# Optimization experiments

Hardware: AMD Instinct MI355X
Metric: run time of the kernel (lower is better)

## Reference

```python
import jax, jax.numpy as jnp
import numpy as np

NEG = -1e9  # finite stand-in for -inf so vjp stays NaN-free
BLANK = 28


def setup_inputs() -> dict:
    key = jax.random.key(0)
    k = jax.random.split(key, 6)
    B, T, D, V, L = 64, 1000, 512, 29, 200
    features = jax.random.normal(k[0], (B, T, D), jnp.float32)
    W = jax.random.normal(k[1], (D, V), jnp.float32) / np.sqrt(D)
    b = jnp.zeros((V,), jnp.float32)
    labels = jax.random.randint(k[2], (B, L), 0, BLANK)          # targets never use blank id
    feature_lengths = jax.random.randint(k[3], (B,), T // 2, T + 1)
    label_lengths = jax.random.randint(k[4], (B,), 50, L + 1)
    return dict(features=features, W=W, b=b, labels=labels,
                feature_lengths=feature_lengths, label_lengths=label_lengths)


def _ctc_loss(log_probs, labels, feature_lengths, label_lengths):
    # log_probs: [T, B, V] (already log_softmax'd)
    T, B, V = log_probs.shape
    L = labels.shape[1]
    S = 2 * L + 1  # extended label length (blanks interleaved)
    ext = jnp.full((B, S), BLANK, labels.dtype).at[:, 1::2].set(labels)  # [B,S]
    # skip transition s-2 -> s allowed iff ext[s] != blank and ext[s] != ext[s-2]
    ext_m2 = jnp.pad(ext[:, :-2], ((0, 0), (2, 0)), constant_values=BLANK)
    allow_skip = (ext != BLANK) & (ext != ext_m2)  # [B,S]
    # gather per-timestep log-probs of extended labels: [T,B,S]
    lp_ext = jnp.take_along_axis(log_probs, jnp.broadcast_to(ext[None], (T, B, S)), axis=2)
    # alpha trellis, t = 0
    alpha = (jnp.full((B, S), NEG, log_probs.dtype)
             .at[:, 0].set(lp_ext[0, :, 0])
             .at[:, 1].set(lp_ext[0, :, 1]))

    def step(alpha, inp):
        lp_t, t = inp  # lp_t: [B,S]
        a2 = jnp.pad(alpha[:, :-1], ((0, 0), (1, 0)), constant_values=NEG)
        a3 = jnp.where(allow_skip,
                       jnp.pad(alpha[:, :-2], ((0, 0), (2, 0)), constant_values=NEG),
                       NEG)
        new = lp_t + jnp.logaddexp(jnp.logaddexp(alpha, a2), a3)
        # freeze alpha once past this sample's input length
        new = jnp.where(t < feature_lengths[:, None], new, alpha)
        return new, None

    alpha, _ = jax.lax.scan(step, alpha, (lp_ext[1:], jnp.arange(1, T)))
    # final states: last blank (2*L_b) and last label (2*L_b - 1)
    idx_blank = 2 * label_lengths  # [B]
    l1 = jnp.take_along_axis(alpha, idx_blank[:, None], axis=1)[:, 0]
    l2 = jnp.take_along_axis(alpha, jnp.maximum(idx_blank - 1, 0)[:, None], axis=1)[:, 0]
    l2 = jnp.where(label_lengths > 0, l2, NEG)
    nll = -jnp.logaddexp(l1, l2)  # [B]
    # PyTorch reduction='mean': divide each loss by target length, then average.
    # zero_infinity=True: infeasible (effectively infinite) losses are zeroed.
    denom = jnp.maximum(label_lengths, 1).astype(log_probs.dtype)
    nll = jnp.where(nll < -0.5 * NEG, nll / denom, 0.0)
    return jnp.mean(nll)


def reference(features, W, b, labels, feature_lengths, label_lengths):
    # model head: Linear(D -> V), then log_softmax and (B,T,V) -> (T,B,V)
    logits = jnp.einsum('btd,dv->btv', features, W) + b
    log_probs = jax.nn.log_softmax(logits, axis=-1).transpose(1, 0, 2)
    return _ctc_loss(log_probs, labels, feature_lengths, label_lengths)
```

## Files before the change

### kernel.cpp

```cpp
#include <hip/hip_runtime.h>
#include <hip/hip_bf16.h>
#include <math.h>

#define B_  64
#define T_  1000
#define D_  512
#define V_  29
#define L_  200
#define S_  401
#define VPAD 32
#define BLANK_ 28

typedef __attribute__((ext_vector_type(8))) short short8v;
typedef __attribute__((ext_vector_type(4))) float float4v;

__device__ __forceinline__ unsigned short f2bf(float f) {
    unsigned int u = __float_as_uint(f);
    return (unsigned short)((u + 0x7FFFu + ((u >> 16) & 1u)) >> 16);
}

__global__ __launch_bounds__(256) void head_mfma_softmax_kernel(
    const float* __restrict__ feat,
    const float* __restrict__ W,
    const float* __restrict__ bias,
    const int*   __restrict__ flen,
    float*       __restrict__ p)
{
    __shared__ uint4 bfrag_lds[16 * 2 * 64];
    const int tid = threadIdx.x;

    for (int f = tid; f < 2048; f += 256) {
        int ks  = f >> 7;
        int rem = f & 127;
        int tl  = rem >> 6;
        int ln  = rem & 63;
        int k0  = ks * 32 + (ln >> 4) * 8;
        int col = tl * 16 + (ln & 15);
        unsigned short h[8];
        #pragma unroll
        for (int j = 0; j < 8; ++j) {
            float wv = (col < V_) ? W[(size_t)(k0 + j) * V_ + col] : 0.f;
            h[j] = f2bf(wv);
        }
        uint4 pk;
        pk.x = h[0] | ((unsigned)h[1] << 16);
        pk.y = h[2] | ((unsigned)h[3] << 16);
        pk.z = h[4] | ((unsigned)h[5] << 16);
        pk.w = h[6] | ((unsigned)h[7] << 16);
        bfrag_lds[f] = pk;
    }
    __syncthreads();

    const int wv  = tid >> 6;
    const int l   = tid & 63;
    const int c0  = l & 15;
    const int grp = l >> 4;
    const float bias0 = bias[c0];
    const bool  v1ok  = (c0 + 16) < V_;
    const float bias1 = v1ok ? bias[c0 + 16] : 0.f;

    #pragma unroll
    for (int ti = 0; ti < 2; ++ti) {
        const int tile = (blockIdx.x * 4 + wv) * 2 + ti;
        const int r0   = tile * 16;
        const int b0 = r0 / T_;
        const bool active = ((r0 - b0 * T_) < flen[b0]) || ((r0 + 15) / T_ != b0);
        if (!active) continue;

        const float* abase = feat + (size_t)(r0 + c0) * D_ + grp * 8;
        float4v acc0 = {0.f, 0.f, 0.f, 0.f};
        float4v acc1 = {0.f, 0.f, 0.f, 0.f};

        #pragma unroll 4
        for (int ks = 0; ks < 16; ++ks) {
            float4 fa = *(const float4*)(abase + ks * 32);
            float4 fb = *(const float4*)(abase + ks * 32 + 4);
            short8v a;
            a[0] = (short)f2bf(fa.x); a[1] = (short)f2bf(fa.y);
            a[2] = (short)f2bf(fa.z); a[3] = (short)f2bf(fa.w);
            a[4] = (short)f2bf(fb.x); a[5] = (short)f2bf(fb.y);
            a[6] = (short)f2bf(fb.z); a[7] = (short)f2bf(fb.w);
            uint4 b0v = bfrag_lds[(ks * 2 + 0) * 64 + l];
            uint4 b1v = bfrag_lds[(ks * 2 + 1) * 64 + l];
            acc0 = __builtin_amdgcn_mfma_f32_16x16x32_bf16(
                       a, __builtin_bit_cast(short8v, b0v), acc0, 0, 0, 0);
            acc1 = __builtin_amdgcn_mfma_f32_16x16x32_bf16(
                       a, __builtin_bit_cast(short8v, b1v), acc1, 0, 0, 0);
        }

        #pragma unroll
        for (int j = 0; j < 4; ++j) {
            float lg0 = acc0[j] + bias0;
            float lg1 = v1ok ? (acc1[j] + bias1) : -1e30f;
            float m = fmaxf(lg0, lg1);
            #pragma unroll
            for (int off = 1; off <= 8; off <<= 1)
                m = fmaxf(m, __shfl_xor(m, off));
            float e0 = __expf(lg0 - m);
            float e1 = v1ok ? __expf(lg1 - m) : 0.f;
            float s = e0 + e1;
            #pragma unroll
            for (int off = 1; off <= 8; off <<= 1)
                s += __shfl_xor(s, off);
            float invs = 1.f / s;
            int r = r0 + grp * 4 + j;
            p[(size_t)r * VPAD + c0]      = e0 * invs;
            p[(size_t)r * VPAD + c0 + 16] = e1 * invs;
        }
    }
}

__device__ __forceinline__ float wave_shr1_zero(float x) {
    return __int_as_float(__builtin_amdgcn_update_dpp(
        0, __float_as_int(x), 0x138 , 0xf, 0xf, true));
}
__device__ __forceinline__ int shr1_self_i(int x) {
    return __builtin_amdgcn_update_dpp(x, x, 0x138 , 0xf, 0xf, false);
}

#define TWO60  1.152921504606846976e18f
#define TWOM60 8.673617379884035e-19f
#define NEGLOG2 (-1.5e9f)

#define CTC_STEP(Q) do {                                                      \
    int   cp = shr1_self_i(c);                                                \
    float u1 = wave_shr1_zero(r[6]);                                          \
    float u2 = wave_shr1_zero(r[5]);                                          \
    int   cm = (c > cp) ? c : cp;                                             \
    int   dc = c  - cm; if (dc < -127) dc = -127;                             \
    int   dp = cp - cm; if (dp < -127) dp = -127;                             \
    float fs = __int_as_float((dc + 127) << 23);                              \
    float fu = __int_as_float((dp + 127) << 23);                              \
    u1 *= fu; u2 *= fu;                                                       \
    float s0 = r[0]*fs, s1 = r[1]*fs, s2 = r[2]*fs, s3 = r[3]*fs;             \
    float s4 = r[4]*fs, s5 = r[5]*fs, s6 = r[6]*fs;                           \
    float n0 = Q[0] * (s0 + u1 + allowf[0] * u2);                             \
    float n1 = Q[1] * (s1 + s0 + allowf[1] * u1);                             \
    float n2 = Q[2] * (s2 + s1 + allowf[2] * s0);                             \
    float n3 = Q[3] * (s3 + s2 + allowf[3] * s1);                             \
    float n4 = Q[4] * (s4 + s3 + allowf[4] * s2);                             \
    float n5 = Q[5] * (s5 + s4 + allowf[5] * s3);                             \
    float n6 = Q[6] * (s6 + s5 + allowf[6] * s4);                             \
    float m  = fmaxf(fmaxf(fmaxf(n0, n1), fmaxf(n2, n3)),                     \
                     fmaxf(fmaxf(n4, n5), n6));                               \
    m = fmaxf(m, TWOM60);                                                     \
    int e   = (__float_as_int(m) >> 23) - 127;            \
    float sc = __int_as_float((187 - e) << 23);          \
    r[0]=n0*sc; r[1]=n1*sc; r[2]=n2*sc; r[3]=n3*sc;                           \
    r[4]=n4*sc; r[5]=n5*sc; r[6]=n6*sc;                                       \
    c = cm + e - 60;                                                          \
} while (0)

#define PREFETCH(Q, row) do {                                                 \
    int _base = (row) * VPAD;                                                 \
    Q[0]=plds[_base+oi[0]]; Q[1]=plds[_base+oi[1]]; Q[2]=plds[_base+oi[2]];   \
    Q[3]=plds[_base+oi[3]]; Q[4]=plds[_base+oi[4]]; Q[5]=plds[_base+oi[5]];   \
    Q[6]=plds[_base+oi[6]];                                                   \
} while (0)

__global__ __launch_bounds__(256) void ctc_alpha_lds_kernel(
    const float* __restrict__ p,
    const int*   __restrict__ labels,
    const int*   __restrict__ flen,
    const int*   __restrict__ llen,
    float*       __restrict__ nll)
{
    __shared__ float plds[T_ * VPAD];
    const int b   = blockIdx.x;
    const int tid = threadIdx.x;
    const float* pb = p + (size_t)b * T_ * VPAD;
    const int Tb = flen[b];
    const int ll = llen[b];

    {
        const float4* src4 = (const float4*)pb;
        float4* dst4 = (float4*)plds;
        const int n4 = Tb * (VPAD / 4);
        for (int i = tid; i < n4; i += 256) dst4[i] = src4[i];
    }
    __syncthreads();

    if (tid < 64) {
        const int lane = tid;

        int   oi[7];
        float allowf[7];
        #pragma unroll
        for (int k = 0; k < 7; ++k) {
            int s = 7 * lane + k;
            int o = 29;
            float al = 0.f;
            if (s < S_) {
                if (s & 1) {
                    int li = (s - 1) >> 1;
                    o = labels[b * L_ + li];
                    if (s >= 3) al = (o != labels[b * L_ + li - 1]) ? 1.f : 0.f;
                } else {
                    o = BLANK_;
                }
            }
            oi[k]     = o;
            allowf[k] = al;
        }

        float r[7];
        int   c = -60;
        {
            float q0[7];
            PREFETCH(q0, 0);
            #pragma unroll
            for (int k = 0; k < 7; ++k)
                r[k] = (lane == 0 && k < 2) ? q0[k] * TWO60 : 0.f;
        }

        float qA[7], qB[7], qN1[7], qN2[7];
        PREFETCH(qA, 1);
        PREFETCH(qB, 2);
        const int Tbm1 = Tb - 1;

        int t = 1;
        for (; t + 1 < Tb; t += 2) {
            int rowA = t + 2; if (rowA > Tbm1) rowA = Tbm1;
            int rowB = t + 3; if (rowB > Tbm1) rowB = Tbm1;
            PREFETCH(qN1, rowA);
            CTC_STEP(qA);
            PREFETCH(qN2, rowB);
            CTC_STEP(qB);
            #pragma unroll
            for (int k = 0; k < 7; ++k) { qA[k] = qN1[k]; qB[k] = qN2[k]; }
        }
        if (t < Tb) CTC_STEP(qA);

        #pragma unroll
        for (int k = 0; k < 7; ++k) {
            float v = r[k];
            plds[7 * lane + k] = (v > 0.f) ? ((float)c + log2f(v)) : NEGLOG2;
        }
    }
    __syncthreads();

    if (tid == 0) {
        int ib = 2 * ll;
        float l1 = plds[ib];
        float l2 = (ll > 0) ? plds[ib - 1] : NEGLOG2;
        float mm = fmaxf(l1, l2);
        float s2 = exp2f(l1 - mm) + exp2f(l2 - mm);
        float nl = -0.6931471805599453f * (mm + log2f(s2));
        nll[b] = (nl < 5e8f) ? nl / fmaxf((float)ll, 1.f) : 0.f;
    }
}

__global__ __launch_bounds__(64) void reduce_mean_kernel(
    const float* __restrict__ nll, float* __restrict__ out)
{
    float v = nll[threadIdx.x];
    #pragma unroll
    for (int off = 32; off; off >>= 1) v += __shfl_down(v, off);
    if (threadIdx.x == 0) out[0] = v * (1.0f / (float)B_);
}

extern "C" void kernel_launch(void* const* d_in, const int* in_sizes, int n_in,
                              void* d_out, int out_size, void* d_ws, size_t ws_size,
                              hipStream_t stream) {
    const float* feat   = (const float*)d_in[0];
    const float* W      = (const float*)d_in[1];
    const float* bias   = (const float*)d_in[2];
    const int*   labels = (const int*)  d_in[3];
    const int*   flen   = (const int*)  d_in[4];
    const int*   llen   = (const int*)  d_in[5];
    float* out = (float*)d_out;

    float* p   = (float*)d_ws;
    float* nll = (float*)((char*)d_ws + (size_t)8 * 1024 * 1024);

    head_mfma_softmax_kernel<<<500, 256, 0, stream>>>(feat, W, bias, flen, p);
    ctc_alpha_lds_kernel<<<B_, 256, 0, stream>>>(p, labels, flen, llen, nll);
    reduce_mean_kernel<<<1, 64, 0, stream>>>(nll, out);
}
```

Baseline: 361.4 us.

## Interleave two CTC sequences per wave and stage probabilities in two halves

The alpha kernel now runs two batch samples per workgroup in one wavefront, interleaving their independent recurrences so each step's dependent latency chain is hidden by the other sample's work. LDS is split into two half-length buffers loaded in two phases (first 500 rows, then the rest), because two full-length buffers would not fit. It launches 32 workgroups instead of 64, which halves parallelism and makes each pair wait for its longer sequence. Frozen steps past a sample's length are masked with selects.

```diff
diff --git a/kernel.cpp b/kernel.cpp
--- a/kernel.cpp
+++ b/kernel.cpp
@@ -10,6 +10,7 @@
 #define S_  401
 #define VPAD 32
 #define BLANK_ 28
+#define HROWS 500
 
 typedef __attribute__((ext_vector_type(8))) short short8v;
 typedef __attribute__((ext_vector_type(4))) float float4v;
@@ -122,131 +123,206 @@
 #define TWOM60 8.673617379884035e-19f
 #define NEGLOG2 (-1.5e9f)
 
-#define CTC_STEP(Q) do {                                                      \
-    int   cp = shr1_self_i(c);                                                \
-    float u1 = wave_shr1_zero(r[6]);                                          \
-    float u2 = wave_shr1_zero(r[5]);                                          \
-    int   cm = (c > cp) ? c : cp;                                             \
-    int   dc = c  - cm; if (dc < -127) dc = -127;                             \
+#define CTC_STEP(rr, cc, Q, alw, act) do {                                    \
+    int   cp = shr1_self_i(cc);                                               \
+    float u1 = wave_shr1_zero(rr[6]);                                         \
+    float u2 = wave_shr1_zero(rr[5]);                                         \
+    int   cm = (cc > cp) ? cc : cp;                                           \
+    int   dc = cc - cm; if (dc < -127) dc = -127;                             \
     int   dp = cp - cm; if (dp < -127) dp = -127;                             \
     float fs = __int_as_float((dc + 127) << 23);                              \
     float fu = __int_as_float((dp + 127) << 23);                              \
     u1 *= fu; u2 *= fu;                                                       \
-    float s0 = r[0]*fs, s1 = r[1]*fs, s2 = r[2]*fs, s3 = r[3]*fs;             \
-    float s4 = r[4]*fs, s5 = r[5]*fs, s6 = r[6]*fs;                           \
-    float n0 = Q[0] * (s0 + u1 + allowf[0] * u2);                             \
-    float n1 = Q[1] * (s1 + s0 + allowf[1] * u1);                             \
-    float n2 = Q[2] * (s2 + s1 + allowf[2] * s0);                             \
-    float n3 = Q[3] * (s3 + s2 + allowf[3] * s1);                             \
-    float n4 = Q[4] * (s4 + s3 + allowf[4] * s2);                             \
-    float n5 = Q[5] * (s5 + s4 + allowf[5] * s3);                             \
-    float n6 = Q[6] * (s6 + s5 + allowf[6] * s4);                             \
+    float s0 = rr[0]*fs, s1 = rr[1]*fs, s2 = rr[2]*fs, s3 = rr[3]*fs;         \
+    float s4 = rr[4]*fs, s5 = rr[5]*fs, s6 = rr[6]*fs;                        \
+    float n0 = Q[0] * (s0 + u1 + alw[0] * u2);                                \
+    float n1 = Q[1] * (s1 + s0 + alw[1] * u1);                                \
+    float n2 = Q[2] * (s2 + s1 + alw[2] * s0);                                \
+    float n3 = Q[3] * (s3 + s2 + alw[3] * s1);                                \
+    float n4 = Q[4] * (s4 + s3 + alw[4] * s2);                                \
+    float n5 = Q[5] * (s5 + s4 + alw[5] * s3);                                \
+    float n6 = Q[6] * (s6 + s5 + alw[6] * s4);                                \
     float m  = fmaxf(fmaxf(fmaxf(n0, n1), fmaxf(n2, n3)),                     \
                      fmaxf(fmaxf(n4, n5), n6));                               \
     m = fmaxf(m, TWOM60);                                                     \
     int e   = (__float_as_int(m) >> 23) - 127;            \
     float sc = __int_as_float((187 - e) << 23);          \
-    r[0]=n0*sc; r[1]=n1*sc; r[2]=n2*sc; r[3]=n3*sc;                           \
-    r[4]=n4*sc; r[5]=n5*sc; r[6]=n6*sc;                                       \
-    c = cm + e - 60;                                                          \
+    rr[0] = (act) ? n0*sc : rr[0];  rr[1] = (act) ? n1*sc : rr[1];            \
+    rr[2] = (act) ? n2*sc : rr[2];  rr[3] = (act) ? n3*sc : rr[3];            \
+    rr[4] = (act) ? n4*sc : rr[4];  rr[5] = (act) ? n5*sc : rr[5];            \
+    rr[6] = (act) ? n6*sc : rr[6];                                            \
+    cc = (act) ? (cm + e - 60) : cc;                                          \
 } while (0)
 
-#define PREFETCH(Q, row) do {                                                 \
-    int _base = (row) * VPAD;                                                 \
-    Q[0]=plds[_base+oi[0]]; Q[1]=plds[_base+oi[1]]; Q[2]=plds[_base+oi[2]];   \
-    Q[3]=plds[_base+oi[3]]; Q[4]=plds[_base+oi[4]]; Q[5]=plds[_base+oi[5]];   \
-    Q[6]=plds[_base+oi[6]];                                                   \
+#define PREFETCH(Q, base, rowoff, oi) do {                                    \
+    int _ba = (rowoff) * VPAD;                                                \
+    Q[0]=base[_ba+oi[0]]; Q[1]=base[_ba+oi[1]]; Q[2]=base[_ba+oi[2]];         \
+    Q[3]=base[_ba+oi[3]]; Q[4]=base[_ba+oi[4]]; Q[5]=base[_ba+oi[5]];         \
+    Q[6]=base[_ba+oi[6]];                                                     \
 } while (0)
 
-__global__ __launch_bounds__(256) void ctc_alpha_lds_kernel(
+#define SETUP_TRELLIS(oi, alw, bb) do {                                       \
+    _Pragma("unroll")                                                         \
+    for (int k = 0; k < 7; ++k) {                                             \
+        int s = 7 * lane + k;                                                 \
+        int o = 29;                   \
+        float al = 0.f;                                                       \
+        if (s < S_) {                                                         \
+            if (s & 1) {                                                      \
+                int li = (s - 1) >> 1;                                        \
+                o = labels[(bb) * L_ + li];                                   \
+                if (s >= 3) al = (o != labels[(bb) * L_ + li - 1]) ? 1.f:0.f; \
+            } else { o = BLANK_; }                                            \
+        }                                                                     \
+        oi[k] = o; alw[k] = al;                                               \
+    }                                                                         \
+} while (0)
+
+__global__ __launch_bounds__(256) void ctc_alpha_lds2_kernel(
     const float* __restrict__ p,
     const int*   __restrict__ labels,
     const int*   __restrict__ flen,
     const int*   __restrict__ llen,
     float*       __restrict__ nll)
 {
-    __shared__ float plds[T_ * VPAD];
-    const int b   = blockIdx.x;
+    __shared__ float ldsA[HROWS * VPAD];
+    __shared__ float ldsB[HROWS * VPAD];
+    const int bA  = blockIdx.x;
+    const int bB  = blockIdx.x + 32;
     const int tid = threadIdx.x;
-    const float* pb = p + (size_t)b * T_ * VPAD;
-    const int Tb = flen[b];
-    const int ll = llen[b];
+    const float* pA = p + (size_t)bA * T_ * VPAD;
+    const float* pB = p + (size_t)bB * T_ * VPAD;
+    const int TbA = flen[bA], TbB = flen[bB];
+    const int mTb = (TbA > TbB) ? TbA : TbB;
 
     {
-        const float4* src4 = (const float4*)pb;
-        float4* dst4 = (float4*)plds;
-        const int n4 = Tb * (VPAD / 4);
-        for (int i = tid; i < n4; i += 256) dst4[i] = src4[i];
-    }
-    __syncthreads();
+        const float4* sA = (const float4*)pA;
+        const float4* sB = (const float4*)pB;
+        float4* dA = (float4*)ldsA;
+        float4* dB = (float4*)ldsB;
+        for (int i = tid; i < HROWS * (VPAD / 4); i += 256) {
+            dA[i] = sA[i];
+            dB[i] = sB[i];
+        }
+    }
+    __syncthreads();
+
+    int   oiA[7], oiB[7];
+    float alwA[7], alwB[7];
+    float rA[7], rB[7];
+    int   cA = -60, cB = -60;
+    float qAA[7], qBA[7], qN1A[7], qN2A[7];
+    float qAB[7], qBB[7], qN1B[7], qN2B[7];
+    const int lane = tid;
 
     if (tid < 64) {
-        const int lane = tid;
-
-        int   oi[7];
-        float allowf[7];
+        SETUP_TRELLIS(oiA, alwA, bA);
+        SETUP_TRELLIS(oiB, alwB, bB);
+
+        {
+            float q0[7];
+            PREFETCH(q0, ldsA, 0, oiA);
+            #pragma unroll
+            for (int k = 0; k < 7; ++k)
+                rA[k] = (lane == 0 && k < 2) ? q0[k] * TWO60 : 0.f;
+            PREFETCH(q0, ldsB, 0, oiB);
+            #pragma unroll
+            for (int k = 0; k < 7; ++k)
+                rB[k] = (lane == 0 && k < 2) ? q0[k] * TWO60 : 0.f;
+        }
+
+        PREFETCH(qAA, ldsA, 1, oiA);  PREFETCH(qAB, ldsB, 1, oiB);
+        PREFETCH(qBA, ldsA, 2, oiA);  PREFETCH(qBB, ldsB, 2, oiB);
+        int t = 1;
+        for (; t + 1 < HROWS; t += 2) {
+            int ro1 = t + 2; if (ro1 > HROWS - 1) ro1 = HROWS - 1;
+            int ro2 = t + 3; if (ro2 > HROWS - 1) ro2 = HROWS - 1;
+            PREFETCH(qN1A, ldsA, ro1, oiA);
+            PREFETCH(qN1B, ldsB, ro1, oiB);
+            CTC_STEP(rA, cA, qAA, alwA, true);
+            CTC_STEP(rB, cB, qAB, alwB, true);
+            PREFETCH(qN2A, ldsA, ro2, oiA);
+            PREFETCH(qN2B, ldsB, ro2, oiB);
+            CTC_STEP(rA, cA, qBA, alwA, true);
+            CTC_STEP(rB, cB, qBB, alwB, true);
+            #pragma unroll
+            for (int k = 0; k < 7; ++k) {
+                qAA[k] = qN1A[k]; qBA[k] = qN2A[k];
+                qAB[k] = qN1B[k]; qBB[k] = qN2B[k];
+            }
+        }
+        CTC_STEP(rA, cA, qAA, alwA, true);
+        CTC_STEP(rB, cB, qAB, alwB, true);
+    }
+    __syncthreads();
+
+    {
+        const float4* sA = (const float4*)(pA + HROWS * VPAD);
+        const float4* sB = (const float4*)(pB + HROWS * VPAD);
+        float4* dA = (float4*)ldsA;
+        float4* dB = (float4*)ldsB;
+        const int nA4 = (TbA - HROWS) * (VPAD / 4);
+        const int nB4 = (TbB - HROWS) * (VPAD / 4);
+        const int n4  = (nA4 > nB4) ? nA4 : nB4;
+        for (int i = tid; i < n4; i += 256) {
+            if (i < nA4) dA[i] = sA[i];
+            if (i < nB4) dB[i] = sB[i];
+        }
+    }
+    __syncthreads();
+
+    if (tid < 64) {
+        if (mTb > HROWS) {
+            PREFETCH(qAA, ldsA, 0, oiA);  PREFETCH(qAB, ldsB, 0, oiB);
+            PREFETCH(qBA, ldsA, 1, oiA);  PREFETCH(qBB, ldsB, 1, oiB);
+            int t = HROWS;
+            for (; t + 1 < mTb; t += 2) {
+                int ro1 = t + 2 - HROWS; if (ro1 > HROWS - 1) ro1 = HROWS - 1;
+                int ro2 = t + 3 - HROWS; if (ro2 > HROWS - 1) ro2 = HROWS - 1;
+                PREFETCH(qN1A, ldsA, ro1, oiA);
+                PREFETCH(qN1B, ldsB, ro1, oiB);
+                CTC_STEP(rA, cA, qAA, alwA, (t < TbA));
+                CTC_STEP(rB, cB, qAB, alwB, (t < TbB));
+                PREFETCH(qN2A, ldsA, ro2, oiA);
+                PREFETCH(qN2B, ldsB, ro2, oiB);
+                CTC_STEP(rA, cA, qBA, alwA, (t + 1 < TbA));
+                CTC_STEP(rB, cB, qBB, alwB, (t + 1 < TbB));
+                #pragma unroll
+                for (int k = 0; k < 7; ++k) {
+                    qAA[k] = qN1A[k]; qBA[k] = qN2A[k];
+                    qAB[k] = qN1B[k]; qBB[k] = qN2B[k];
+                }
+            }
+            if (t < mTb) {
+                CTC_STEP(rA, cA, qAA, alwA, (t < TbA));
+                CTC_STEP(rB, cB, qAB, alwB, (t < TbB));
+            }
+        }
+
         #pragma unroll
         for (int k = 0; k < 7; ++k) {
-            int s = 7 * lane + k;
-            int o = 29;
-            float al = 0.f;
-            if (s < S_) {
-                if (s & 1) {
-                    int li = (s - 1) >> 1;
-                    o = labels[b * L_ + li];
-                    if (s >= 3) al = (o != labels[b * L_ + li - 1]) ? 1.f : 0.f;
-                } else {
-                    o = BLANK_;
-                }
-            }
-            oi[k]     = o;
-            allowf[k] = al;
-        }
-
-        float r[7];
-        int   c = -60;
-        {
-            float q0[7];
-            PREFETCH(q0, 0);
-            #pragma unroll
-            for (int k = 0; k < 7; ++k)
-                r[k] = (lane == 0 && k < 2) ? q0[k] * TWO60 : 0.f;
-        }
-
-        float qA[7], qB[7], qN1[7], qN2[7];
-        PREFETCH(qA, 1);
-        PREFETCH(qB, 2);
-        const int Tbm1 = Tb - 1;
-
-        int t = 1;
-        for (; t + 1 < Tb; t += 2) {
-            int rowA = t + 2; if (rowA > Tbm1) rowA = Tbm1;
-            int rowB = t + 3; if (rowB > Tbm1) rowB = Tbm1;
-            PREFETCH(qN1, rowA);
-            CTC_STEP(qA);
-            PREFETCH(qN2, rowB);
-            CTC_STEP(qB);
-            #pragma unroll
-            for (int k = 0; k < 7; ++k) { qA[k] = qN1[k]; qB[k] = qN2[k]; }
-        }
-        if (t < Tb) CTC_STEP(qA);
-
+            float vA = rA[k];
+            ldsA[7 * lane + k] = (vA > 0.f) ? ((float)cA + log2f(vA)) : NEGLOG2;
+            float vB = rB[k];
+            ldsB[7 * lane + k] = (vB > 0.f) ? ((float)cB + log2f(vB)) : NEGLOG2;
+        }
+    }
+    __syncthreads();
+
+    if (tid == 0) {
         #pragma unroll
-        for (int k = 0; k < 7; ++k) {
-            float v = r[k];
-            plds[7 * lane + k] = (v > 0.f) ? ((float)c + log2f(v)) : NEGLOG2;
-        }
-    }
-    __syncthreads();
-
-    if (tid == 0) {
-        int ib = 2 * ll;
-        float l1 = plds[ib];
-        float l2 = (ll > 0) ? plds[ib - 1] : NEGLOG2;
-        float mm = fmaxf(l1, l2);
-        float s2 = exp2f(l1 - mm) + exp2f(l2 - mm);
-        float nl = -0.6931471805599453f * (mm + log2f(s2));
-        nll[b] = (nl < 5e8f) ? nl / fmaxf((float)ll, 1.f) : 0.f;
+        for (int which = 0; which < 2; ++which) {
+            const float* fin = which ? ldsB : ldsA;
+            const int bb = which ? bB : bA;
+            const int ll = llen[bb];
+            int ib = 2 * ll;
+            float l1 = fin[ib];
+            float l2 = (ll > 0) ? fin[ib - 1] : NEGLOG2;
+            float mm = fmaxf(l1, l2);
+            float s2 = exp2f(l1 - mm) + exp2f(l2 - mm);
+            float nl = -0.6931471805599453f * (mm + log2f(s2));
+            nll[bb] = (nl < 5e8f) ? nl / fmaxf((float)ll, 1.f) : 0.f;
+        }
     }
 }
 
@@ -274,6 +350,6 @@
     float* nll = (float*)((char*)d_ws + (size_t)8 * 1024 * 1024);
 
     head_mfma_softmax_kernel<<<500, 256, 0, stream>>>(feat, W, bias, flen, p);
-    ctc_alpha_lds_kernel<<<B_, 256, 0, stream>>>(p, labels, flen, llen, nll);
+    ctc_alpha_lds2_kernel<<<32, 256, 0, stream>>>(p, labels, flen, llen, nll);
     reduce_mean_kernel<<<1, 64, 0, stream>>>(nll, out);
 }
```

Measured after the change: 492.3 us. 1.36x slower.
